# Performance work log

Measured on AMD Instinct MI355X. Metric: run time of the kernel, lower is better.

Reference implementation:

```python
import jax, jax.numpy as jnp
import numpy as np

NEG = jnp.float32(-1e30)


def setup_inputs() -> dict:
    key = jax.random.key(0)
    k1, k2, k3, k4 = jax.random.split(key, 4)
    B, T, K, Dmax = 16, 2048, 256, 64
    # per-timestep emission log-likelihoods (would come from self.pdf.log_prob(X))
    log_B = jax.random.normal(k1, (B, T, K), dtype=jnp.float32)
    # normalized log-prob buffers, matching _init_buffers (Dirichlet-ish -> log_softmax)
    pi_logits = jax.nn.log_softmax(jax.random.normal(k2, (K,), dtype=jnp.float32))
    # SEMI transition constraint: no self transitions (diagonal = -inf), rows normalized
    A_raw = jax.random.normal(k3, (K, K), dtype=jnp.float32)
    A_raw = jnp.where(jnp.eye(K, dtype=bool), NEG, A_raw)
    A_logits = jax.nn.log_softmax(A_raw, axis=1)
    D_logits = jax.nn.log_softmax(jax.random.normal(k4, (K, Dmax), dtype=jnp.float32), axis=1)
    return {"log_B": log_B, "pi_logits": pi_logits, "A_logits": A_logits, "D_logits": D_logits}


def _hsmm_forward(logb, cumb, pi_logits, A_logits, D_logits):
    """Explicit-duration HSMM forward pass (log-space) for one sequence.

    alpha_t(j) = logsumexp_{d=1..Dmax} [ a_{t-d}(j) + D_j(d) + sum_{s=t-d+1..t} b_j(o_s) ]
    a_tau(j)   = logsumexp_i alpha_tau(i) + A_{ij},  a_0 = pi.
    Segment emission sums via cumsum: cumb[t] - cumb[t-d].
    Carry a rolling buffer buf[d-1, j] = a_{t-d}(j) - cumb[t-d](j).
    """
    K = pi_logits.shape[0]
    Dmax = D_logits.shape[1]
    Dt = D_logits.T  # [Dmax, K]
    # t=1: only d=1 valid, buf[0] = a_0 - cumb[0] = pi - 0
    buf0 = jnp.full((Dmax, K), NEG, dtype=logb.dtype).at[0].set(pi_logits)

    def step(buf, cumb_t):
        # alpha_t(j): logsumexp over durations d
        alpha = jax.nn.logsumexp(buf + Dt, axis=0) + cumb_t          # [K]
        # incoming mass for a segment starting at t+1
        a_in = jax.nn.logsumexp(alpha[:, None] + A_logits, axis=0)   # [K]
        buf = jnp.roll(buf, 1, axis=0).at[0].set(a_in - cumb_t)
        return buf, alpha

    _, alphas = jax.lax.scan(step, buf0, cumb)  # alphas: [T, K]
    loglik = jax.nn.logsumexp(alphas[-1])
    return loglik, alphas


def reference(log_B, pi_logits, A_logits, D_logits):
    cumB = jnp.cumsum(log_B, axis=1)  # [B, T, K]
    loglik, alphas = jax.vmap(_hsmm_forward, in_axes=(0, 0, None, None, None))(
        log_B, cumB, pi_logits, A_logits, D_logits)
    return loglik, alphas
```

## Files before the change

### kernel.cpp

```cpp
#include <hip/hip_runtime.h>
#include <cstddef>

#define LOG2E 1.4426950408889634f
#define LN2   0.6931471805599453f

typedef float    f32x2 __attribute__((ext_vector_type(2)));
typedef float    f32x4 __attribute__((ext_vector_type(4)));
typedef _Float16 half8 __attribute__((ext_vector_type(8)));

constexpr int K_    = 256;
constexpr int T_    = 2048;
constexpr int DMAX_ = 64;
constexpr int B_    = 16;

__device__ __forceinline__ float fexp2(float x) { return __builtin_amdgcn_exp2f(x); }
__device__ __forceinline__ float flog2(float x) { return __builtin_amdgcn_logf(x); }
__device__ __forceinline__ float frcp (float x) { return __builtin_amdgcn_rcpf(x); }

__device__ __forceinline__ f32x2 xchg32(float x) {
    float a = x, b;
    asm("v_mov_b32 %1, %2\n\t"
        "s_nop 1\n\t"
        "v_permlane32_swap_b32 %0, %1"
        : "+v"(a), "=&v"(b)
        : "v"(x));
    return (f32x2){a, b};
}

template<int CTRL>
__device__ __forceinline__ float dpp_maxf(float x) {
    int m = __builtin_amdgcn_update_dpp(0, __builtin_bit_cast(int, x), CTRL, 0xF, 0xF, true);
    return fmaxf(x, __builtin_bit_cast(float, m));
}

__global__ __launch_bounds__(512)
__attribute__((amdgpu_waves_per_eu(2, 2)))
void hsmm_fwd_kernel(const float* __restrict__ logB,
                     const float* __restrict__ pi,
                     const float* __restrict__ A,
                     const float* __restrict__ D,
                     float* __restrict__ out)
{
    const int b    = blockIdx.x;
    const int tid  = threadIdx.x;
    const int w    = tid >> 6;
    const int lane = tid & 63;
    const int j    = (w << 5) | (lane & 31);
    const int q    = lane >> 5;

    alignas(16) __shared__ _Float16 lds_ph[2][K_];
    alignas(16) __shared__ float    lds_red[8];

    half8 Bf0[8], Bf1[8];
    {
        const int krow = (lane >> 4) * 8;
        const int n0   = (w << 5) + (lane & 15);
        #pragma unroll
        for (int kc = 0; kc < 8; ++kc) {
            #pragma unroll
            for (int jj = 0; jj < 8; ++jj) {
                const int k = kc * 32 + krow + jj;
                Bf0[kc][jj] = (_Float16)fexp2(A[(size_t)k * K_ + n0     ] * LOG2E);
                Bf1[kc][jj] = (_Float16)fexp2(A[(size_t)k * K_ + n0 + 16] * LOG2E);
            }
        }
    }
    f32x2 pDf[16];
    {
        const float* Dj = D + (size_t)j * DMAX_ + 32 * q;
        #pragma unroll
        for (int i = 0; i < 16; ++i)
            pDf[i] = (f32x2){ fexp2(Dj[i] * LOG2E), fexp2(Dj[16 + i] * LOG2E) };
    }

    f32x2 v[16];
    #pragma unroll
    for (int i = 0; i < 16; ++i) v[i] = (f32x2){0.0f, 0.0f};
    if (q == 0) v[0].x = 1.0f;
    float mcol     = pi[j] * LOG2E;
    float cumb     = 0.0f;
    float m_anchor = 0.0f;

    if (tid < 8) lds_red[tid] = 0.0f;
    __syncthreads();

    const float* lb = logB + (size_t)b * T_ * K_ + j;
    float*       ao = out + 16 + (size_t)b * T_ * K_ + j;

    float bld0 = lb[0];
    float bld1 = lb[K_];
    float bld2 = lb[2 * K_];
    int   ldoff = 3 * K_;
    int   aoff  = 0;

    auto body = [&](int t, int s, bool even) __attribute__((always_inline)) {
        cumb = fmaf(bld0, LOG2E, cumb);

        const float argh = 0.5f * (cumb + mcol - m_anchor);
        const float ea   = fminf(fexp2(argh),  1.8e19f);
        const float ga   = fminf(fexp2(-argh), 1.8e19f);
        const float mac  = m_anchor - cumb;

        f32x2 s0 = {0.f,0.f}, s1 = {0.f,0.f}, s2 = {0.f,0.f}, s3 = {0.f,0.f};
        #pragma unroll
        for (int k = 0; k < 16; k += 4) {
            s0 = __builtin_elementwise_fma(v[k + 0], pDf[k + 0], s0);
            s1 = __builtin_elementwise_fma(v[k + 1], pDf[k + 1], s1);
            s2 = __builtin_elementwise_fma(v[k + 2], pDf[k + 2], s2);
            s3 = __builtin_elementwise_fma(v[k + 3], pDf[k + 3], s3);
        }
        f32x2 sp = (s0 + s1) + (s2 + s3);
        float Sl = sp.x + sp.y;
        f32x2 pr = xchg32(Sl);
        float S  = pr.x + pr.y;

        float p = fminf(S * ea * ea, 60000.0f);
        if (q == 0) lds_ph[s][j] = (_Float16)p;

        asm volatile("s_waitcnt lgkmcnt(0)" ::: "memory");
        __builtin_amdgcn_sched_barrier(0);
        __builtin_amdgcn_s_barrier();
        __builtin_amdgcn_sched_barrier(0);

        bld0 = bld1; bld1 = bld2;
        bld2 = lb[ldoff];
        ldoff += (ldoff < (T_ - 1) * K_) ? K_ : 0;
        if (q == 0) ao[aoff] = (cumb + mcol + flog2(S)) * LN2;
        aoff += K_;

        f32x4 r0, r1;
        if (!even) {
            r0 = ((const f32x4*)lds_red)[0];
            r1 = ((const f32x4*)lds_red)[1];
        }

        const _Float16* pb = lds_ph[s];
        const int fo = (lane >> 4) * 8;
        const f32x4 z = {0.f,0.f,0.f,0.f};
        f32x4 d0a = z, d0b = z, d1a = z, d1b = z;
        #pragma unroll
        for (int kc = 0; kc < 4; ++kc) {
            half8 af = *(const half8*)(pb + kc * 32 + fo);
            d0a = __builtin_amdgcn_mfma_f32_16x16x32_f16(af, Bf0[kc], d0a, 0, 0, 0);
            d1a = __builtin_amdgcn_mfma_f32_16x16x32_f16(af, Bf1[kc], d1a, 0, 0, 0);
        }
        #pragma unroll
        for (int kc = 4; kc < 8; ++kc) {
            half8 af = *(const half8*)(pb + kc * 32 + fo);
            d0b = __builtin_amdgcn_mfma_f32_16x16x32_f16(af, Bf0[kc], d0b, 0, 0, 0);
            d1b = __builtin_amdgcn_mfma_f32_16x16x32_f16(af, Bf1[kc], d1b, 0, 0, 0);
        }
        float sva = d0a.x + d0b.x;
        float svb = d1a.x + d1b.x;
        float mySmv = (lane & 16) ? svb : sva;

        float m_next = 0.0f;
        if (even) {
            float mx = fmaxf(sva, svb);
            mx = dpp_maxf<0x121>(mx);
            mx = dpp_maxf<0x122>(mx);
            mx = dpp_maxf<0x124>(mx);
            mx = dpp_maxf<0x128>(mx);
            if (lane == 0) lds_red[w] = m_anchor + flog2(fmaxf(mx, 1e-30f));
        } else {
            float m1 = fmaxf(fmaxf(r0.x, r0.y), fmaxf(r0.z, r0.w));
            float m2 = fmaxf(fmaxf(r1.x, r1.y), fmaxf(r1.z, r1.w));
            m_next = fmaxf(m1, m2);
        }

        float nv0 = mySmv * ga * ga;
        float rsc = frcp(fmaxf(nv0, 1.0f));
        float nv  = fminf(nv0, 1.0f);
        mcol = fmaxf(mcol, mac + flog2(mySmv));

        f32x2 hp  = xchg32(v[15].y);
        float oth = (hp.x == v[15].y) ? hp.y : hp.x;
        float p15lo = v[15].x;
        f32x2 rp = { rsc, rsc };
        #pragma unroll
        for (int k = 15; k >= 1; --k)
            v[k] = v[k - 1] * rp;
        v[0].y = p15lo * rsc;
        v[0].x = (q == 0) ? nv : oth * rsc;

        if (!even && t + 1 < T_) m_anchor = m_next;
    };

    for (int t = 0; t < T_; t += 2) {
        body(t,     0, true );
        body(t + 1, 1, false);
    }

    if (tid < 64) {
        const _Float16* lp = lds_ph[(T_ - 1) & 1];
        float sf = (float)lp[tid] + (float)lp[tid + 64]
                 + (float)lp[tid + 128] + (float)lp[tid + 192];
        #pragma unroll
        for (int off = 1; off < 64; off <<= 1)
            sf += __shfl_xor(sf, off, 64);
        if (tid == 0) out[b] = (m_anchor + flog2(sf)) * LN2;
    }
}

extern "C" void kernel_launch(void* const* d_in, const int* in_sizes, int n_in,
                              void* d_out, int out_size, void* d_ws, size_t ws_size,
                              hipStream_t stream) {
    const float* logB = (const float*)d_in[0];
    const float* pi   = (const float*)d_in[1];
    const float* A    = (const float*)d_in[2];
    const float* D    = (const float*)d_in[3];
    float* out = (float*)d_out;
    (void)in_sizes; (void)n_in; (void)d_ws; (void)ws_size; (void)out_size;

    hipLaunchKernelGGL(hsmm_fwd_kernel, dim3(B_), dim3(512), 0, stream,
                       logB, pi, A, D, out);
}
```

Before: 1.440 ms.

## Split each state across four lane groups using 1024-thread blocks

Each block grows from 512 to 1024 threads. Each wave now owns 16 states instead of 32, and each state's duration buffer is split across four 16-lane groups instead of two. That halves per-thread registers and halves the MFMA work per wave, with one 16x16 tile instead of two. The duration reduction adds a permlane16 swap, the buffer shift across groups uses ds_bpermute, and the max reduction reads 16 LDS entries. The aim is to shorten the serial per-timestep critical path. The cost is more waves hitting the barrier each step and an extra LDS permute in the recurrence.

```diff
diff --git a/kernel.cpp b/kernel.cpp
--- a/kernel.cpp
+++ b/kernel.cpp
@@ -27,14 +27,29 @@
     return (f32x2){a, b};
 }
 
+__device__ __forceinline__ f32x2 xchg16(float x) {
+    float a = x, b;
+    asm("v_mov_b32 %1, %2\n\t"
+        "s_nop 1\n\t"
+        "v_permlane16_swap_b32 %0, %1"
+        : "+v"(a), "=&v"(b)
+        : "v"(x));
+    return (f32x2){a, b};
+}
+
+__device__ __forceinline__ float bpermf(int addr, float v) {
+    return __builtin_bit_cast(float,
+        __builtin_amdgcn_ds_bpermute(addr, __builtin_bit_cast(int, v)));
+}
+
 template<int CTRL>
 __device__ __forceinline__ float dpp_maxf(float x) {
     int m = __builtin_amdgcn_update_dpp(0, __builtin_bit_cast(int, x), CTRL, 0xF, 0xF, true);
     return fmaxf(x, __builtin_bit_cast(float, m));
 }
 
-__global__ __launch_bounds__(512)
-__attribute__((amdgpu_waves_per_eu(2, 2)))
+__global__ __launch_bounds__(1024)
+__attribute__((amdgpu_waves_per_eu(4, 4)))
 void hsmm_fwd_kernel(const float* __restrict__ logB,
                      const float* __restrict__ pi,
                      const float* __restrict__ A,
@@ -45,43 +60,43 @@
     const int tid  = threadIdx.x;
     const int w    = tid >> 6;
     const int lane = tid & 63;
-    const int j    = (w << 5) | (lane & 31);
-    const int q    = lane >> 5;
+    const int j    = (w << 4) | (lane & 15);
+    const int g    = lane >> 4;
 
     alignas(16) __shared__ _Float16 lds_ph[2][K_];
-    alignas(16) __shared__ float    lds_red[8];
-
-    half8 Bf0[8], Bf1[8];
+    alignas(16) __shared__ float    lds_red[16];
+
+    half8 Bf[8];
     {
-        const int krow = (lane >> 4) * 8;
-        const int n0   = (w << 5) + (lane & 15);
+        const int krow = g * 8;
         #pragma unroll
         for (int kc = 0; kc < 8; ++kc) {
             #pragma unroll
             for (int jj = 0; jj < 8; ++jj) {
                 const int k = kc * 32 + krow + jj;
-                Bf0[kc][jj] = (_Float16)fexp2(A[(size_t)k * K_ + n0     ] * LOG2E);
-                Bf1[kc][jj] = (_Float16)fexp2(A[(size_t)k * K_ + n0 + 16] * LOG2E);
+                Bf[kc][jj] = (_Float16)fexp2(A[(size_t)k * K_ + j] * LOG2E);
             }
         }
     }
-    f32x2 pDf[16];
+    f32x2 pDf[8];
     {
-        const float* Dj = D + (size_t)j * DMAX_ + 32 * q;
-        #pragma unroll
-        for (int i = 0; i < 16; ++i)
-            pDf[i] = (f32x2){ fexp2(Dj[i] * LOG2E), fexp2(Dj[16 + i] * LOG2E) };
-    }
-
-    f32x2 v[16];
+        const float* Dj = D + (size_t)j * DMAX_ + 16 * g;
+        #pragma unroll
+        for (int i = 0; i < 8; ++i)
+            pDf[i] = (f32x2){ fexp2(Dj[i] * LOG2E), fexp2(Dj[8 + i] * LOG2E) };
+    }
+
+    f32x2 v[8];
     #pragma unroll
-    for (int i = 0; i < 16; ++i) v[i] = (f32x2){0.0f, 0.0f};
-    if (q == 0) v[0].x = 1.0f;
+    for (int i = 0; i < 8; ++i) v[i] = (f32x2){0.0f, 0.0f};
+    if (g == 0) v[0].x = 1.0f;
     float mcol     = pi[j] * LOG2E;
     float cumb     = 0.0f;
     float m_anchor = 0.0f;
 
-    if (tid < 8) lds_red[tid] = 0.0f;
+    const int bpa = ((lane - 16) & 63) << 2;
+
+    if (tid < 16) lds_red[tid] = 0.0f;
     __syncthreads();
 
     const float* lb = logB + (size_t)b * T_ * K_ + j;
@@ -102,20 +117,23 @@
         const float mac  = m_anchor - cumb;
 
         f32x2 s0 = {0.f,0.f}, s1 = {0.f,0.f}, s2 = {0.f,0.f}, s3 = {0.f,0.f};
-        #pragma unroll
-        for (int k = 0; k < 16; k += 4) {
-            s0 = __builtin_elementwise_fma(v[k + 0], pDf[k + 0], s0);
-            s1 = __builtin_elementwise_fma(v[k + 1], pDf[k + 1], s1);
-            s2 = __builtin_elementwise_fma(v[k + 2], pDf[k + 2], s2);
-            s3 = __builtin_elementwise_fma(v[k + 3], pDf[k + 3], s3);
-        }
+        s0 = __builtin_elementwise_fma(v[0], pDf[0], s0);
+        s1 = __builtin_elementwise_fma(v[1], pDf[1], s1);
+        s2 = __builtin_elementwise_fma(v[2], pDf[2], s2);
+        s3 = __builtin_elementwise_fma(v[3], pDf[3], s3);
+        s0 = __builtin_elementwise_fma(v[4], pDf[4], s0);
+        s1 = __builtin_elementwise_fma(v[5], pDf[5], s1);
+        s2 = __builtin_elementwise_fma(v[6], pDf[6], s2);
+        s3 = __builtin_elementwise_fma(v[7], pDf[7], s3);
         f32x2 sp = (s0 + s1) + (s2 + s3);
         float Sl = sp.x + sp.y;
-        f32x2 pr = xchg32(Sl);
-        float S  = pr.x + pr.y;
+        f32x2 q16 = xchg16(Sl);
+        float Sq  = q16.x + q16.y;
+        f32x2 pr  = xchg32(Sq);
+        float S   = pr.x + pr.y;
 
         float p = fminf(S * ea * ea, 60000.0f);
-        if (q == 0) lds_ph[s][j] = (_Float16)p;
+        if (lane < 16) lds_ph[s][j] = (_Float16)p;
 
         asm volatile("s_waitcnt lgkmcnt(0)" ::: "memory");
         __builtin_amdgcn_sched_barrier(0);
@@ -125,38 +143,36 @@
         bld0 = bld1; bld1 = bld2;
         bld2 = lb[ldoff];
         ldoff += (ldoff < (T_ - 1) * K_) ? K_ : 0;
-        if (q == 0) ao[aoff] = (cumb + mcol + flog2(S)) * LN2;
+        if (lane < 16) ao[aoff] = (cumb + mcol + flog2(S)) * LN2;
         aoff += K_;
 
-        f32x4 r0, r1;
+        f32x4 r0, r1, r2, r3;
         if (!even) {
             r0 = ((const f32x4*)lds_red)[0];
             r1 = ((const f32x4*)lds_red)[1];
+            r2 = ((const f32x4*)lds_red)[2];
+            r3 = ((const f32x4*)lds_red)[3];
         }
 
         const _Float16* pb = lds_ph[s];
-        const int fo = (lane >> 4) * 8;
+        const int fo = g * 8;
         const f32x4 z = {0.f,0.f,0.f,0.f};
-        f32x4 d0a = z, d0b = z, d1a = z, d1b = z;
+        f32x4 d0a = z, d0b = z;
         #pragma unroll
         for (int kc = 0; kc < 4; ++kc) {
             half8 af = *(const half8*)(pb + kc * 32 + fo);
-            d0a = __builtin_amdgcn_mfma_f32_16x16x32_f16(af, Bf0[kc], d0a, 0, 0, 0);
-            d1a = __builtin_amdgcn_mfma_f32_16x16x32_f16(af, Bf1[kc], d1a, 0, 0, 0);
+            d0a = __builtin_amdgcn_mfma_f32_16x16x32_f16(af, Bf[kc], d0a, 0, 0, 0);
         }
         #pragma unroll
         for (int kc = 4; kc < 8; ++kc) {
             half8 af = *(const half8*)(pb + kc * 32 + fo);
-            d0b = __builtin_amdgcn_mfma_f32_16x16x32_f16(af, Bf0[kc], d0b, 0, 0, 0);
-            d1b = __builtin_amdgcn_mfma_f32_16x16x32_f16(af, Bf1[kc], d1b, 0, 0, 0);
-        }
-        float sva = d0a.x + d0b.x;
-        float svb = d1a.x + d1b.x;
-        float mySmv = (lane & 16) ? svb : sva;
+            d0b = __builtin_amdgcn_mfma_f32_16x16x32_f16(af, Bf[kc], d0b, 0, 0, 0);
+        }
+        float mySmv = d0a.x + d0b.x;
 
         float m_next = 0.0f;
         if (even) {
-            float mx = fmaxf(sva, svb);
+            float mx = mySmv;
             mx = dpp_maxf<0x121>(mx);
             mx = dpp_maxf<0x122>(mx);
             mx = dpp_maxf<0x124>(mx);
@@ -165,7 +181,9 @@
         } else {
             float m1 = fmaxf(fmaxf(r0.x, r0.y), fmaxf(r0.z, r0.w));
             float m2 = fmaxf(fmaxf(r1.x, r1.y), fmaxf(r1.z, r1.w));
-            m_next = fmaxf(m1, m2);
+            float m3 = fmaxf(fmaxf(r2.x, r2.y), fmaxf(r2.z, r2.w));
+            float m4 = fmaxf(fmaxf(r3.x, r3.y), fmaxf(r3.z, r3.w));
+            m_next = fmaxf(fmaxf(m1, m2), fmaxf(m3, m4));
         }
 
         float nv0 = mySmv * ga * ga;
@@ -173,15 +191,14 @@
         float nv  = fminf(nv0, 1.0f);
         mcol = fmaxf(mcol, mac + flog2(mySmv));
 
-        f32x2 hp  = xchg32(v[15].y);
-        float oth = (hp.x == v[15].y) ? hp.y : hp.x;
-        float p15lo = v[15].x;
+        float oth = bpermf(bpa, v[7].y);
+        float p7x = v[7].x;
         f32x2 rp = { rsc, rsc };
         #pragma unroll
-        for (int k = 15; k >= 1; --k)
+        for (int k = 7; k >= 1; --k)
             v[k] = v[k - 1] * rp;
-        v[0].y = p15lo * rsc;
-        v[0].x = (q == 0) ? nv : oth * rsc;
+        v[0].y = p7x * rsc;
+        v[0].x = (g == 0) ? nv : oth * rsc;
 
         if (!even && t + 1 < T_) m_anchor = m_next;
     };
@@ -212,6 +229,6 @@
     float* out = (float*)d_out;
     (void)in_sizes; (void)n_in; (void)d_ws; (void)ws_size; (void)out_size;
 
-    hipLaunchKernelGGL(hsmm_fwd_kernel, dim3(B_), dim3(512), 0, stream,
+    hipLaunchKernelGGL(hsmm_fwd_kernel, dim3(B_), dim3(1024), 0, stream,
                        logB, pi, A, D, out);
 }
```

Measured after the change: 1.804 ms. 25.3% more time.

## Process two sequences per block, sharing MFMA transition matmul across batch rows

Applied to the files above, without the earlier changes.

Each block now runs two batch sequences together. The per-step transition product uses MFMA rows for both sequences at once, with zero-filled rows in LDS padding the unused rows, so the otherwise idle MFMA rows carry the second sequence. Duration recurrences and max reductions are duplicated per sequence, and exp(-x) is replaced by a reciprocal. This halves the grid to 8 blocks and removes half the barriers in exchange for more ALU work and register pressure in each serial step.

```diff
diff --git a/kernel.cpp b/kernel.cpp
--- a/kernel.cpp
+++ b/kernel.cpp
@@ -41,15 +41,17 @@
                      const float* __restrict__ D,
                      float* __restrict__ out)
 {
-    const int b    = blockIdx.x;
+    const int blk  = blockIdx.x;
+    const int bA   = blk << 1, bB = bA | 1;
     const int tid  = threadIdx.x;
     const int w    = tid >> 6;
     const int lane = tid & 63;
     const int j    = (w << 5) | (lane & 31);
     const int q    = lane >> 5;
 
-    alignas(16) __shared__ _Float16 lds_ph[2][K_];
-    alignas(16) __shared__ float    lds_red[8];
+    alignas(16) __shared__ _Float16 lds_p[2][512];
+    alignas(16) __shared__ _Float16 lds_z[256];
+    alignas(16) __shared__ float    lds_red[16];
 
     half8 Bf0[8], Bf1[8];
     {
@@ -73,132 +75,171 @@
             pDf[i] = (f32x2){ fexp2(Dj[i] * LOG2E), fexp2(Dj[16 + i] * LOG2E) };
     }
 
-    f32x2 v[16];
+    f32x2 vA[16], vB[16];
     #pragma unroll
-    for (int i = 0; i < 16; ++i) v[i] = (f32x2){0.0f, 0.0f};
-    if (q == 0) v[0].x = 1.0f;
-    float mcol     = pi[j] * LOG2E;
-    float cumb     = 0.0f;
-    float m_anchor = 0.0f;
-
-    if (tid < 8) lds_red[tid] = 0.0f;
+    for (int i = 0; i < 16; ++i) { vA[i] = (f32x2){0.f,0.f}; vB[i] = (f32x2){0.f,0.f}; }
+    if (q == 0) { vA[0].x = 1.0f; vB[0].x = 1.0f; }
+    float mcA = pi[j] * LOG2E, mcB = mcA;
+    float cbA = 0.0f, cbB = 0.0f;
+    float maA = 0.0f, maB = 0.0f;
+
+    const int sel = lane & 3;
+    const int fo  = (lane >> 4) * 8;
+    const _Float16* a0 = (sel == 0) ? &lds_p[0][fo]
+                       : (sel == 1) ? &lds_p[0][256 + fo] : &lds_z[fo];
+    const _Float16* a1 = (sel == 0) ? &lds_p[1][fo]
+                       : (sel == 1) ? &lds_p[1][256 + fo] : &lds_z[fo];
+    _Float16* wp0 = &lds_p[0][(q << 8) + j];
+    _Float16* wp1 = &lds_p[1][(q << 8) + j];
+
+    if (tid < 16)  lds_red[tid] = 0.0f;
+    if (tid < 256) lds_z[tid]   = (_Float16)0.0f;
     __syncthreads();
 
-    const float* lb = logB + (size_t)b * T_ * K_ + j;
-    float*       ao = out + 16 + (size_t)b * T_ * K_ + j;
-
-    float bld0 = lb[0];
-    float bld1 = lb[K_];
-    float bld2 = lb[2 * K_];
+    const float* lbA = logB + (size_t)bA * T_ * K_ + j;
+    const float* lbB = logB + (size_t)bB * T_ * K_ + j;
+    float*       aoP = out + 16 + (size_t)(q ? bB : bA) * T_ * K_ + j;
+
+    float fA0 = lbA[0], fA1 = lbA[K_], fA2 = lbA[2 * K_];
+    float fB0 = lbB[0], fB1 = lbB[K_], fB2 = lbB[2 * K_];
     int   ldoff = 3 * K_;
     int   aoff  = 0;
 
-    auto body = [&](int t, int s, bool even) __attribute__((always_inline)) {
-        cumb = fmaf(bld0, LOG2E, cumb);
-
-        const float argh = 0.5f * (cumb + mcol - m_anchor);
-        const float ea   = fminf(fexp2(argh),  1.8e19f);
-        const float ga   = fminf(fexp2(-argh), 1.8e19f);
-        const float mac  = m_anchor - cumb;
-
-        f32x2 s0 = {0.f,0.f}, s1 = {0.f,0.f}, s2 = {0.f,0.f}, s3 = {0.f,0.f};
-        #pragma unroll
-        for (int k = 0; k < 16; k += 4) {
-            s0 = __builtin_elementwise_fma(v[k + 0], pDf[k + 0], s0);
-            s1 = __builtin_elementwise_fma(v[k + 1], pDf[k + 1], s1);
-            s2 = __builtin_elementwise_fma(v[k + 2], pDf[k + 2], s2);
-            s3 = __builtin_elementwise_fma(v[k + 3], pDf[k + 3], s3);
-        }
-        f32x2 sp = (s0 + s1) + (s2 + s3);
-        float Sl = sp.x + sp.y;
-        f32x2 pr = xchg32(Sl);
-        float S  = pr.x + pr.y;
-
-        float p = fminf(S * ea * ea, 60000.0f);
-        if (q == 0) lds_ph[s][j] = (_Float16)p;
+    auto body = [&](int s, bool even, bool upd) __attribute__((always_inline)) {
+        cbA = fmaf(fA0, LOG2E, cbA);
+        cbB = fmaf(fB0, LOG2E, cbB);
+
+        const float exA = fexp2(0.5f * (cbA + mcA - maA));
+        const float eaA = fminf(exA, 1.8e19f), gaA = fminf(frcp(exA), 1.8e19f);
+        const float mmA = maA - cbA;
+        const float exB = fexp2(0.5f * (cbB + mcB - maB));
+        const float eaB = fminf(exB, 1.8e19f), gaB = fminf(frcp(exB), 1.8e19f);
+        const float mmB = maB - cbB;
+
+        f32x2 t0={0.f,0.f}, t1={0.f,0.f}, t2={0.f,0.f}, t3={0.f,0.f};
+        f32x2 u0={0.f,0.f}, u1={0.f,0.f}, u2={0.f,0.f}, u3={0.f,0.f};
+        #pragma unroll
+        for (int i = 0; i < 16; i += 4) {
+            t0 = __builtin_elementwise_fma(vA[i + 0], pDf[i + 0], t0);
+            t1 = __builtin_elementwise_fma(vA[i + 1], pDf[i + 1], t1);
+            t2 = __builtin_elementwise_fma(vA[i + 2], pDf[i + 2], t2);
+            t3 = __builtin_elementwise_fma(vA[i + 3], pDf[i + 3], t3);
+            u0 = __builtin_elementwise_fma(vB[i + 0], pDf[i + 0], u0);
+            u1 = __builtin_elementwise_fma(vB[i + 1], pDf[i + 1], u1);
+            u2 = __builtin_elementwise_fma(vB[i + 2], pDf[i + 2], u2);
+            u3 = __builtin_elementwise_fma(vB[i + 3], pDf[i + 3], u3);
+        }
+        f32x2 spA = (t0 + t1) + (t2 + t3);
+        f32x2 spB = (u0 + u1) + (u2 + u3);
+        f32x2 prA = xchg32(spA.x + spA.y);
+        f32x2 prB = xchg32(spB.x + spB.y);
+        const float SA = prA.x + prA.y;
+        const float SB = prB.x + prB.y;
+
+        const float pAv = fminf(SA * eaA * eaA, 60000.0f);
+        const float pBv = fminf(SB * eaB * eaB, 60000.0f);
+        (s ? wp1 : wp0)[0] = (_Float16)(q ? pBv : pAv);
 
         asm volatile("s_waitcnt lgkmcnt(0)" ::: "memory");
         __builtin_amdgcn_sched_barrier(0);
         __builtin_amdgcn_s_barrier();
         __builtin_amdgcn_sched_barrier(0);
 
-        bld0 = bld1; bld1 = bld2;
-        bld2 = lb[ldoff];
+        fA0 = fA1; fA1 = fA2; fA2 = lbA[ldoff];
+        fB0 = fB1; fB1 = fB2; fB2 = lbB[ldoff];
         ldoff += (ldoff < (T_ - 1) * K_) ? K_ : 0;
-        if (q == 0) ao[aoff] = (cumb + mcol + flog2(S)) * LN2;
+        aoP[aoff] = q ? (cbB + mcB + flog2(SB)) * LN2
+                      : (cbA + mcA + flog2(SA)) * LN2;
         aoff += K_;
 
-        f32x4 r0, r1;
+        f32x4 r0, r1, r2, r3;
         if (!even) {
             r0 = ((const f32x4*)lds_red)[0];
             r1 = ((const f32x4*)lds_red)[1];
-        }
-
-        const _Float16* pb = lds_ph[s];
-        const int fo = (lane >> 4) * 8;
+            r2 = ((const f32x4*)lds_red)[2];
+            r3 = ((const f32x4*)lds_red)[3];
+        }
+
+        const _Float16* pb = s ? a1 : a0;
         const f32x4 z = {0.f,0.f,0.f,0.f};
         f32x4 d0a = z, d0b = z, d1a = z, d1b = z;
         #pragma unroll
         for (int kc = 0; kc < 4; ++kc) {
-            half8 af = *(const half8*)(pb + kc * 32 + fo);
+            half8 af = *(const half8*)(pb + kc * 32);
             d0a = __builtin_amdgcn_mfma_f32_16x16x32_f16(af, Bf0[kc], d0a, 0, 0, 0);
             d1a = __builtin_amdgcn_mfma_f32_16x16x32_f16(af, Bf1[kc], d1a, 0, 0, 0);
         }
         #pragma unroll
         for (int kc = 4; kc < 8; ++kc) {
-            half8 af = *(const half8*)(pb + kc * 32 + fo);
+            half8 af = *(const half8*)(pb + kc * 32);
             d0b = __builtin_amdgcn_mfma_f32_16x16x32_f16(af, Bf0[kc], d0b, 0, 0, 0);
             d1b = __builtin_amdgcn_mfma_f32_16x16x32_f16(af, Bf1[kc], d1b, 0, 0, 0);
         }
-        float sva = d0a.x + d0b.x;
-        float svb = d1a.x + d1b.x;
-        float mySmv = (lane & 16) ? svb : sva;
-
-        float m_next = 0.0f;
+        const float s0x = d0a.x + d0b.x, s1x = d1a.x + d1b.x;
+        const float s0y = d0a.y + d0b.y, s1y = d1a.y + d1b.y;
+        const float smA = (lane & 16) ? s1x : s0x;
+        const float smB = (lane & 16) ? s1y : s0y;
+
+        float mnA = 0.0f, mnB = 0.0f;
         if (even) {
-            float mx = fmaxf(sva, svb);
-            mx = dpp_maxf<0x121>(mx);
-            mx = dpp_maxf<0x122>(mx);
-            mx = dpp_maxf<0x124>(mx);
-            mx = dpp_maxf<0x128>(mx);
-            if (lane == 0) lds_red[w] = m_anchor + flog2(fmaxf(mx, 1e-30f));
+            float mxA = fmaxf(s0x, s1x), mxB = fmaxf(s0y, s1y);
+            mxA = dpp_maxf<0x121>(mxA); mxB = dpp_maxf<0x121>(mxB);
+            mxA = dpp_maxf<0x122>(mxA); mxB = dpp_maxf<0x122>(mxB);
+            mxA = dpp_maxf<0x124>(mxA); mxB = dpp_maxf<0x124>(mxB);
+            mxA = dpp_maxf<0x128>(mxA); mxB = dpp_maxf<0x128>(mxB);
+            if (lane == 0)
+                *(f32x2*)&lds_red[w * 2] = (f32x2){
+                    maA + flog2(fmaxf(mxA, 1e-30f)),
+                    maB + flog2(fmaxf(mxB, 1e-30f)) };
         } else {
-            float m1 = fmaxf(fmaxf(r0.x, r0.y), fmaxf(r0.z, r0.w));
-            float m2 = fmaxf(fmaxf(r1.x, r1.y), fmaxf(r1.z, r1.w));
-            m_next = fmaxf(m1, m2);
-        }
-
-        float nv0 = mySmv * ga * ga;
-        float rsc = frcp(fmaxf(nv0, 1.0f));
-        float nv  = fminf(nv0, 1.0f);
-        mcol = fmaxf(mcol, mac + flog2(mySmv));
-
-        f32x2 hp  = xchg32(v[15].y);
-        float oth = (hp.x == v[15].y) ? hp.y : hp.x;
-        float p15lo = v[15].x;
-        f32x2 rp = { rsc, rsc };
-        #pragma unroll
-        for (int k = 15; k >= 1; --k)
-            v[k] = v[k - 1] * rp;
-        v[0].y = p15lo * rsc;
-        v[0].x = (q == 0) ? nv : oth * rsc;
-
-        if (!even && t + 1 < T_) m_anchor = m_next;
+            mnA = fmaxf(fmaxf(fmaxf(r0.x, r0.z), fmaxf(r1.x, r1.z)),
+                        fmaxf(fmaxf(r2.x, r2.z), fmaxf(r3.x, r3.z)));
+            mnB = fmaxf(fmaxf(fmaxf(r0.y, r0.w), fmaxf(r1.y, r1.w)),
+                        fmaxf(fmaxf(r2.y, r2.w), fmaxf(r3.y, r3.w)));
+        }
+
+        const float n0A = smA * gaA * gaA;
+        const float rsA = frcp(fmaxf(n0A, 1.0f));
+        const float nvA = fminf(n0A, 1.0f);
+        mcA = fmaxf(mcA, mmA + flog2(smA));
+        const float n0B = smB * gaB * gaB;
+        const float rsB = frcp(fmaxf(n0B, 1.0f));
+        const float nvB = fminf(n0B, 1.0f);
+        mcB = fmaxf(mcB, mmB + flog2(smB));
+
+        f32x2 hA = xchg32(vA[15].y);
+        f32x2 hB = xchg32(vB[15].y);
+        const float oA = (hA.x == vA[15].y) ? hA.y : hA.x;
+        const float oB = (hB.x == vB[15].y) ? hB.y : hB.x;
+        const float pxA = vA[15].x, pxB = vB[15].x;
+        const f32x2 rpA = { rsA, rsA }, rpB = { rsB, rsB };
+        #pragma unroll
+        for (int k = 15; k >= 1; --k) {
+            vA[k] = vA[k - 1] * rpA;
+            vB[k] = vB[k - 1] * rpB;
+        }
+        vA[0].y = pxA * rsA;  vA[0].x = (q == 0) ? nvA : oA * rsA;
+        vB[0].y = pxB * rsB;  vB[0].x = (q == 0) ? nvB : oB * rsB;
+
+        if (!even && upd) { maA = mnA; maB = mnB; }
     };
 
     for (int t = 0; t < T_; t += 2) {
-        body(t,     0, true );
-        body(t + 1, 1, false);
-    }
-
-    if (tid < 64) {
-        const _Float16* lp = lds_ph[(T_ - 1) & 1];
-        float sf = (float)lp[tid] + (float)lp[tid + 64]
-                 + (float)lp[tid + 128] + (float)lp[tid + 192];
+        body(0, true,  true);
+        body(1, false, t + 2 < T_);
+    }
+
+    if (tid < 128) {
+        const int g64 = tid >> 6;
+        const _Float16* lp = lds_p[1] + (g64 << 8);
+        const int l6 = tid & 63;
+        float sf = (float)lp[l6] + (float)lp[l6 + 64]
+                 + (float)lp[l6 + 128] + (float)lp[l6 + 192];
         #pragma unroll
         for (int off = 1; off < 64; off <<= 1)
             sf += __shfl_xor(sf, off, 64);
-        if (tid == 0) out[b] = (m_anchor + flog2(sf)) * LN2;
+        if (l6 == 0)
+            out[g64 ? bB : bA] = ((g64 ? maB : maA) + flog2(sf)) * LN2;
     }
 }
 
@@ -212,6 +253,6 @@
     float* out = (float*)d_out;
     (void)in_sizes; (void)n_in; (void)d_ws; (void)ws_size; (void)out_size;
 
-    hipLaunchKernelGGL(hsmm_fwd_kernel, dim3(B_), dim3(512), 0, stream,
+    hipLaunchKernelGGL(hsmm_fwd_kernel, dim3(B_ / 2), dim3(512), 0, stream,
                        logB, pi, A, D, out);
 }
```

Measured after the change: 2.110 ms. 46.6% more time.
